# Kernel tuning notes

Hardware: AMD Instinct MI355X
Metric: run time of the kernel (lower is better)

## Reference

```python
import jax, jax.numpy as jnp
import numpy as np

B, L, HID, NH = 8, 1024, 1024, 16
DH = HID // NH
EPS = 1e-12


def _linear(x, W, b):
    # torch nn.Linear: y = x @ W.T + b
    return jnp.einsum('ble,oe->blo', x, W) + b


def _attend(qx, kx, vx, mask, Wq, bq, Wk, bk, Wv, bv):
    q = _linear(qx, Wq, bq).reshape(B, -1, NH, DH)
    k = _linear(kx, Wk, bk).reshape(B, -1, NH, DH)
    v = _linear(vx, Wv, bv).reshape(B, -1, NH, DH)
    scores = jnp.einsum('bqhd,bkhd->bhqk', q, k) / np.sqrt(DH).astype(np.float32)
    scores = scores + mask  # additive mask broadcast [B,1,1,Lk]
    probs = jax.nn.softmax(scores, axis=-1)  # dropout = identity (eval mode)
    ctx = jnp.einsum('bhqk,bkhd->bqhd', probs, v)
    return ctx.reshape(B, -1, HID)


def _layernorm(x, gamma, beta):
    mu = jnp.mean(x, axis=-1, keepdims=True)
    var = jnp.mean(jnp.square(x - mu), axis=-1, keepdims=True)
    return gamma * (x - mu) * jax.lax.rsqrt(var + EPS) + beta


def setup_inputs():
    key = jax.random.key(0)
    ks = jax.random.split(key, 20)
    s = 0.02
    d = {
        'cinput_tensor': jax.random.normal(ks[0], (B, L, HID), jnp.float32),
        'qinput_tensor': jax.random.normal(ks[1], (B, L, HID), jnp.float32),
        'attention_mask': jnp.zeros((B, 1, 1, L), jnp.float32),
        'qattention_mask': jnp.zeros((B, 1, 1, L), jnp.float32),
    }
    names = ['Wq', 'Wk', 'Wv', 'Wqq', 'Wqk', 'Wqv', 'Wo']
    for i, n in enumerate(names):
        d[n] = jax.random.normal(ks[2 + i], (HID, HID), jnp.float32) * s
        d['b' + n[1:]] = jnp.zeros((HID,), jnp.float32)
    d['gamma'] = jnp.ones((HID,), jnp.float32)
    d['beta'] = jnp.zeros((HID,), jnp.float32)
    return d


def reference(cinput_tensor, qinput_tensor, attention_mask, qattention_mask,
              Wq, bq, Wk, bk, Wv, bv, Wqq, bqq, Wqk, bqk, Wqv, bqv,
              Wo, bo, gamma, beta):
    enc, dec = cinput_tensor, qinput_tensor
    # c-branch: query from dec, key/value from enc
    ctx = _attend(dec, enc, enc, attention_mask, Wq, bq, Wk, bk, Wv, bv)
    # q-branch: query from enc, key/value from dec
    qctx = _attend(enc, dec, dec, qattention_mask, Wqq, bqq, Wqk, bqk, Wqv, bqv)
    # output: same dense/LayerNorm reused, and BOTH residuals add cinput_tensor
    # (faithful to the original module, including its apparent bug)
    c_out = _layernorm(_linear(ctx, Wo, bo) + cinput_tensor, gamma, beta)
    q_out = _layernorm(_linear(qctx, Wo, bo) + cinput_tensor, gamma, beta)
    return (c_out, q_out)
```

## Files before the change

kernel.cpp:

```cpp
#include <hip/hip_runtime.h>

typedef __bf16 bf16;
typedef unsigned short u16;
typedef __bf16 bf16x8 __attribute__((ext_vector_type(8)));
typedef __bf16 bf16x4 __attribute__((ext_vector_type(4)));
typedef float f32x4 __attribute__((ext_vector_type(4)));

#define GLD16(g, l) __builtin_amdgcn_global_load_lds( \
    (const __attribute__((address_space(1))) void*)(g), \
    (__attribute__((address_space(3))) void*)(l), 16, 0, 0)

#define MFMA_BF16 __builtin_amdgcn_mfma_f32_16x16x32_bf16

struct CvtFlat { const float* s[9]; bf16* d[9]; int off[10]; };

__global__ __launch_bounds__(256) void cvt_flat(CvtFlat a) {
  const int g = blockIdx.x * 256 + threadIdx.x;
  int seg = 0;
  #pragma unroll
  for (int i = 1; i < 9; ++i) seg += (g >= a.off[i]) ? 1 : 0;
  const int loc = (g - a.off[seg]) * 4;
  const f32x4 v = *(const f32x4*)(a.s[seg] + loc);
  bf16x4 o;
  #pragma unroll
  for (int j = 0; j < 4; ++j) o[j] = (bf16)v[j];
  *(bf16x4*)(a.d[seg] + loc) = o;
}

struct GemmDesc {
  const bf16* X;
  const bf16* W;
  const float* B;
  const float* R;
  bf16* Y;
  int vt;
};
struct GemmArgs { GemmDesc d[6]; };

__global__ __launch_bounds__(256, 2) void gemm128(GemmArgs args) {
  const GemmDesc g = args.d[blockIdx.z];
  __shared__ u16 As[128 * 64];
  __shared__ u16 Bs[128 * 64];
  const int tid = threadIdx.x;
  const int w = tid >> 6, lane = tid & 63;
  const int lq = lane >> 4, ll = lane & 15;
  const int lin = blockIdx.x + (blockIdx.y << 3);
  const int ntile = (lin >> 3) & 7;
  const int mtile = (lin & 7) | ((lin >> 6) << 3);
  const int m0 = mtile * 128, n0 = ntile * 128;
  const int wm = (w >> 1) * 64, wn = (w & 1) * 64;
  f32x4 acc[4][4] = {};

  for (int k0 = 0; k0 < 1024; k0 += 64) {
    #pragma unroll
    for (int i = 0; i < 4; ++i) {
      const int sb = w * 256 + i * 64;
      const int s = sb + lane;
      const int r = s >> 3, c = (s & 7) ^ (r & 7);
      GLD16(g.X + (m0 + r) * 1024 + k0 + c * 8, &As[sb * 8]);
      GLD16(g.W + (n0 + r) * 1024 + k0 + c * 8, &Bs[sb * 8]);
    }
    __syncthreads();
    #pragma unroll
    for (int kk = 0; kk < 64; kk += 32) {
      const int cb = (kk >> 3) + lq;
      bf16x8 a[4], b[4];
      #pragma unroll
      for (int t = 0; t < 4; ++t) {
        const int m = wm + t * 16 + ll;
        a[t] = *(const bf16x8*)&As[m * 64 + ((cb ^ (m & 7)) << 3)];
        const int n = wn + t * 16 + ll;
        b[t] = *(const bf16x8*)&Bs[n * 64 + ((cb ^ (n & 7)) << 3)];
      }
      #pragma unroll
      for (int mt = 0; mt < 4; ++mt)
        #pragma unroll
        for (int nt = 0; nt < 4; ++nt)
          acc[mt][nt] = MFMA_BF16(a[mt], b[nt], acc[mt][nt], 0, 0, 0);
    }
    __syncthreads();
  }

  float biasv[4];
  #pragma unroll
  for (int nt = 0; nt < 4; ++nt) biasv[nt] = g.B[n0 + wn + nt * 16 + ll];

  #pragma unroll
  for (int mt = 0; mt < 4; ++mt) {
    #pragma unroll
    for (int r = 0; r < 4; ++r) {
      const int m = m0 + wm + mt * 16 + lq * 4 + r;
      #pragma unroll
      for (int nt = 0; nt < 4; ++nt) {
        const int n = n0 + wn + nt * 16 + ll;
        float v = acc[mt][nt][r] + biasv[nt];
        if (g.R) v += g.R[m * 1024 + n];
        if (!g.vt) {
          g.Y[m * 1024 + n] = (bf16)v;
        } else {
          const int bb = m >> 10, tok = m & 1023;
          g.Y[(((bb << 4) + (n >> 6)) * 64 + (n & 63)) * 1024 + tok] = (bf16)v;
        }
      }
    }
  }
}

struct AttnDesc { const bf16* Qp; const bf16* Kp; const bf16* Vt; const float* mask; bf16* ctx; };

__global__ __launch_bounds__(256, 4) void attn_kernel(AttnDesc A0, AttnDesc A1) {
  const AttnDesc A = blockIdx.z ? A1 : A0;
  __shared__ u16 Ks[128 * 64];
  __shared__ u16 Vts[64 * 128];
  __shared__ u16 Pts[4 * 1024];
  const int tid = threadIdx.x;
  const int w = tid >> 6, lane = tid & 63;
  const int lq = lane >> 4, ll = lane & 15;
  const int lin = blockIdx.x + (blockIdx.y << 3);
  const int bh = (lin & 7) | ((lin >> 6) << 3);
  const int q0 = ((lin >> 3) & 7) * 128;
  const int b = bh >> 4, h = bh & 15;
  const float* mrow = A.mask + b * 1024;

  #pragma unroll
  for (int i = 0; i < 4; ++i) {
    const int sb = w * 256 + i * 64;
    const int s = sb + lane;
    const int r = s >> 3, c = (s & 7) ^ (r & 7);
    GLD16(A.Qp + (b * 1024 + q0 + r) * 1024 + h * 64 + c * 8, &Ks[sb * 8]);
  }
  __syncthreads();
  bf16x8 bq[2][2];
  #pragma unroll
  for (int nt = 0; nt < 2; ++nt)
    #pragma unroll
    for (int kd = 0; kd < 2; ++kd) {
      const int row = w * 32 + nt * 16 + ll;
      const int c8 = kd * 4 + lq;
      bq[nt][kd] = *(const bf16x8*)&Ks[row * 64 + ((c8 ^ (row & 7)) << 3)];
    }
  __syncthreads();

  f32x4 oacc[4][2] = {};
  float rsum[2] = {0.f, 0.f};

  for (int kt = 0; kt < 8; ++kt) {
    const int kk0 = kt * 128;
    #pragma unroll
    for (int i = 0; i < 4; ++i) {
      const int sb = w * 256 + i * 64;
      const int s = sb + lane;
      { const int r = s >> 3, c = (s & 7) ^ (r & 7);
        GLD16(A.Kp + (b * 1024 + kk0 + r) * 1024 + h * 64 + c * 8, &Ks[sb * 8]); }
      { const int r = s >> 4, c = (s & 15) ^ (r & 15);
        GLD16(A.Vt + (bh * 64 + r) * 1024 + kk0 + c * 8, &Vts[sb * 8]); }
    }
    __syncthreads();

    #pragma unroll
    for (int qtr = 0; qtr < 4; ++qtr) {
      bf16x8 ak[2][2];
      #pragma unroll
      for (int mh = 0; mh < 2; ++mh) {
        const int row = qtr * 32 + mh * 16 + ll;
        #pragma unroll
        for (int kd = 0; kd < 2; ++kd) {
          const int c8 = kd * 4 + lq;
          ak[mh][kd] = *(const bf16x8*)&Ks[row * 64 + ((c8 ^ (row & 7)) << 3)];
        }
      }
      f32x4 sacc[2][2] = {};
      #pragma unroll
      for (int mh = 0; mh < 2; ++mh)
        #pragma unroll
        for (int nt = 0; nt < 2; ++nt)
          #pragma unroll
          for (int kd = 0; kd < 2; ++kd)
            sacc[mh][nt] = MFMA_BF16(ak[mh][kd], bq[nt][kd], sacc[mh][nt], 0, 0, 0);

      f32x4 mv[2];
      #pragma unroll
      for (int mh = 0; mh < 2; ++mh)
        mv[mh] = *(const f32x4*)&mrow[kk0 + qtr * 32 + mh * 16 + lq * 4];

      #pragma unroll
      for (int mh = 0; mh < 2; ++mh)
        #pragma unroll
        for (int nt = 0; nt < 2; ++nt) {
          bf16x4 pv;
          #pragma unroll
          for (int rr = 0; rr < 4; ++rr) {
            const float p = __expf(fmaf(sacc[mh][nt][rr], 0.125f, mv[mh][rr]));
            rsum[nt] += p;
            pv[rr] = (bf16)p;
          }
          const int row = nt * 16 + ll;
          const int gq = mh * 2 + (lq >> 1);
          *(bf16x4*)&Pts[w * 1024 + row * 32 + ((gq ^ (row & 3)) << 3) + (lq & 1) * 4] = pv;
        }

      bf16x8 bp[2];
      #pragma unroll
      for (int nt = 0; nt < 2; ++nt) {
        const int row = nt * 16 + ll;
        bp[nt] = *(const bf16x8*)&Pts[w * 1024 + row * 32 + ((lq ^ (row & 3)) << 3)];
      }
      #pragma unroll
      for (int mtd = 0; mtd < 4; ++mtd) {
        const int row = mtd * 16 + ll;
        const int c16 = (qtr * 4 + lq) ^ (row & 15);
        const bf16x8 av = *(const bf16x8*)&Vts[row * 128 + (c16 << 3)];
        oacc[mtd][0] = MFMA_BF16(av, bp[0], oacc[mtd][0], 0, 0, 0);
        oacc[mtd][1] = MFMA_BF16(av, bp[1], oacc[mtd][1], 0, 0, 0);
      }
    }
    __syncthreads();
  }

  #pragma unroll
  for (int nt = 0; nt < 2; ++nt) {
    rsum[nt] += __shfl_xor(rsum[nt], 16, 64);
    rsum[nt] += __shfl_xor(rsum[nt], 32, 64);
  }

  #pragma unroll
  for (int nt = 0; nt < 2; ++nt) {
    const float inv = 1.f / rsum[nt];
    const int tok = q0 + w * 32 + nt * 16 + ll;
    #pragma unroll
    for (int mtd = 0; mtd < 4; ++mtd) {
      bf16x4 ov;
      #pragma unroll
      for (int rr = 0; rr < 4; ++rr) ov[rr] = (bf16)(oacc[mtd][nt][rr] * inv);
      *(bf16x4*)&A.ctx[(size_t)(b * 1024 + tok) * 1024 + h * 64 + mtd * 16 + lq * 4] = ov;
    }
  }
}

__global__ __launch_bounds__(256) void ln_kernel(const bf16* __restrict__ pre_c,
                                                 const bf16* __restrict__ pre_q,
                                                 const float* __restrict__ gamma,
                                                 const float* __restrict__ beta,
                                                 float* __restrict__ out) {
  const int row = blockIdx.x;
  const bf16* src = (row < 8192) ? (pre_c + (size_t)row * 1024)
                                 : (pre_q + (size_t)(row - 8192) * 1024);
  float* dst = out + (size_t)row * 1024;
  const int t = threadIdx.x;
  const bf16x4 xv = *(const bf16x4*)(src + t * 4);
  float x[4]; float s = 0.f, ss = 0.f;
  #pragma unroll
  for (int i = 0; i < 4; ++i) { x[i] = (float)xv[i]; s += x[i]; ss += x[i] * x[i]; }
  #pragma unroll
  for (int off = 1; off < 64; off <<= 1) { s += __shfl_xor(s, off, 64); ss += __shfl_xor(ss, off, 64); }
  __shared__ float red[8];
  const int w = t >> 6, lane = t & 63;
  if (lane == 0) { red[w * 2] = s; red[w * 2 + 1] = ss; }
  __syncthreads();
  s  = red[0] + red[2] + red[4] + red[6];
  ss = red[1] + red[3] + red[5] + red[7];
  const float mu = s * (1.f / 1024.f);
  float var = ss * (1.f / 1024.f) - mu * mu;
  var = fmaxf(var, 0.f);
  const float rs = rsqrtf(var + 1e-12f);
  const f32x4 gv = *(const f32x4*)(gamma + t * 4);
  const f32x4 bv = *(const f32x4*)(beta + t * 4);
  f32x4 yv;
  #pragma unroll
  for (int i = 0; i < 4; ++i) yv[i] = gv[i] * (x[i] - mu) * rs + bv[i];
  *(f32x4*)(dst + t * 4) = yv;
}

extern "C" void kernel_launch(void* const* d_in, const int* in_sizes, int n_in,
                              void* d_out, int out_size, void* d_ws, size_t ws_size,
                              hipStream_t stream) {
  const float* enc    = (const float*)d_in[0];
  const float* dec    = (const float*)d_in[1];
  const float* mask_c = (const float*)d_in[2];
  const float* mask_q = (const float*)d_in[3];
  const float* Wq  = (const float*)d_in[4];  const float* bq  = (const float*)d_in[5];
  const float* Wk  = (const float*)d_in[6];  const float* bk  = (const float*)d_in[7];
  const float* Wv  = (const float*)d_in[8];  const float* bv  = (const float*)d_in[9];
  const float* Wqq = (const float*)d_in[10]; const float* bqq = (const float*)d_in[11];
  const float* Wqk = (const float*)d_in[12]; const float* bqk = (const float*)d_in[13];
  const float* Wqv = (const float*)d_in[14]; const float* bqv = (const float*)d_in[15];
  const float* Wo  = (const float*)d_in[16]; const float* bo  = (const float*)d_in[17];
  const float* gamma = (const float*)d_in[18];
  const float* beta  = (const float*)d_in[19];
  float* out = (float*)d_out;

  bf16* ws = (bf16*)d_ws;
  const size_t XSZ = (size_t)8192 * 1024;
  const size_t WSZ = (size_t)1024 * 1024;
  bf16* enc_b = ws;
  bf16* dec_b = enc_b + XSZ;
  bf16* Wb[7];
  for (int i = 0; i < 7; ++i) Wb[i] = dec_b + XSZ + i * WSZ;
  bf16* after_w = Wb[6] + WSZ;

  CvtFlat ca;
  ca.s[0] = enc; ca.d[0] = enc_b;
  ca.s[1] = dec; ca.d[1] = dec_b;
  const float* Wsrc[7] = {Wq, Wk, Wv, Wqq, Wqk, Wqv, Wo};
  for (int i = 0; i < 7; ++i) { ca.s[2 + i] = Wsrc[i]; ca.d[2 + i] = Wb[i]; }
  int running = 0;
  const int segn[9] = {(int)(XSZ / 4), (int)(XSZ / 4), (int)(WSZ / 4), (int)(WSZ / 4),
                       (int)(WSZ / 4), (int)(WSZ / 4), (int)(WSZ / 4), (int)(WSZ / 4), (int)(WSZ / 4)};
  for (int i = 0; i < 9; ++i) { ca.off[i] = running; running += segn[i]; }
  ca.off[9] = running;
  const int cvt_blocks = running / 256;

  const size_t need_par = (size_t)(23 + 48) * 1024 * 1024 * 2;

  cvt_flat<<<dim3(cvt_blocks), 256, 0, stream>>>(ca);

  if (ws_size >= need_par) {
    bf16* Qc  = after_w;        bf16* Kc  = Qc + XSZ;  bf16* Vtc = Kc + XSZ;
    bf16* Qq  = Vtc + XSZ;      bf16* Kq  = Qq + XSZ;  bf16* Vtq = Kq + XSZ;
    bf16* ctx_c = enc_b;
    bf16* ctx_q = dec_b;
    bf16* pre_c = Qc;
    bf16* pre_q = Qq;

    GemmArgs pa = {};
    pa.d[0] = {dec_b, Wb[0], bq,  nullptr, Qc,  0};
    pa.d[1] = {enc_b, Wb[1], bk,  nullptr, Kc,  0};
    pa.d[2] = {enc_b, Wb[2], bv,  nullptr, Vtc, 1};
    pa.d[3] = {enc_b, Wb[3], bqq, nullptr, Qq,  0};
    pa.d[4] = {dec_b, Wb[4], bqk, nullptr, Kq,  0};
    pa.d[5] = {dec_b, Wb[5], bqv, nullptr, Vtq, 1};
    gemm128<<<dim3(8, 64, 6), 256, 0, stream>>>(pa);

    AttnDesc a0 = {Qc, Kc, Vtc, mask_c, ctx_c};
    AttnDesc a1 = {Qq, Kq, Vtq, mask_q, ctx_q};
    attn_kernel<<<dim3(8, 128, 2), 256, 0, stream>>>(a0, a1);

    GemmArgs oa = {};
    oa.d[0] = {ctx_c, Wb[6], bo, enc, pre_c, 0};
    oa.d[1] = {ctx_q, Wb[6], bo, enc, pre_q, 0};
    gemm128<<<dim3(8, 64, 2), 256, 0, stream>>>(oa);

    ln_kernel<<<dim3(16384), 256, 0, stream>>>(pre_c, pre_q, gamma, beta, out);
  } else {
    bf16* Q  = after_w;  bf16* K = Q + XSZ;  bf16* Vt = K + XSZ;
    bf16* ctx_c = Vt + XSZ;
    bf16* ctx_q = ctx_c + XSZ;
    bf16* pre_c = Q;
    bf16* pre_q = K;

    GemmArgs pa = {};
    pa.d[0] = {dec_b, Wb[0], bq,  nullptr, Q,  0};
    pa.d[1] = {enc_b, Wb[1], bk,  nullptr, K,  0};
    pa.d[2] = {enc_b, Wb[2], bv,  nullptr, Vt, 1};
    gemm128<<<dim3(8, 64, 3), 256, 0, stream>>>(pa);

    AttnDesc a0 = {Q, K, Vt, mask_c, ctx_c};
    attn_kernel<<<dim3(8, 128, 1), 256, 0, stream>>>(a0, a0);

    GemmArgs pb = {};
    pb.d[0] = {enc_b, Wb[3], bqq, nullptr, Q,  0};
    pb.d[1] = {dec_b, Wb[4], bqk, nullptr, K,  0};
    pb.d[2] = {dec_b, Wb[5], bqv, nullptr, Vt, 1};
    gemm128<<<dim3(8, 64, 3), 256, 0, stream>>>(pb);

    AttnDesc a1 = {Q, K, Vt, mask_q, ctx_q};
    attn_kernel<<<dim3(8, 128, 1), 256, 0, stream>>>(a1, a1);

    GemmArgs oa = {};
    oa.d[0] = {ctx_c, Wb[6], bo, enc, pre_c, 0};
    oa.d[1] = {ctx_q, Wb[6], bo, enc, pre_q, 0};
    gemm128<<<dim3(8, 64, 2), 256, 0, stream>>>(oa);

    ln_kernel<<<dim3(16384), 256, 0, stream>>>(pre_c, pre_q, gamma, beta, out);
  }
}
```

Before: 484.0 us.

## Replace 128x128 GEMM with 256x256 tile, 4-stage LDS pipelined kernel

Replaces the 128x128, 256-thread GEMM with a 256x256, 512-thread kernel. It uses a 4-slot shared-memory ring of K=32 slices, issuing global-to-LDS loads three slices ahead and interleaving them with MFMA bursts under raw barriers and explicit waitcnt. It also uses s_setprio around the MFMA bursts and a new swizzle and tile ordering. The goal is to hide global load latency and raise operand reuse per loaded byte. The cost is fewer blocks (128 tiles per matrix) with heavy register and LDS use (128KB LDS), which may limit occupancy and tail balance.

```diff
diff --git a/kernel.cpp b/kernel.cpp
--- a/kernel.cpp
+++ b/kernel.cpp
@@ -11,6 +11,9 @@
     (__attribute__((address_space(3))) void*)(l), 16, 0, 0)
 
 #define MFMA_BF16 __builtin_amdgcn_mfma_f32_16x16x32_bf16
+
+#define FENCE() asm volatile("" ::: "memory")
+#define BARRIER() do { FENCE(); __builtin_amdgcn_s_barrier(); FENCE(); } while (0)
 
 struct CvtFlat { const float* s[9]; bf16* d[9]; int off[10]; };
 
@@ -37,62 +40,115 @@
 };
 struct GemmArgs { GemmDesc d[6]; };
 
-__global__ __launch_bounds__(256, 2) void gemm128(GemmArgs args) {
+__device__ __forceinline__ void stage_slice(const bf16* G, int row0, int k0,
+                                            u16* slot, int w, int lane) {
+  #pragma unroll
+  for (int i = 0; i < 2; ++i) {
+    const int sb = i * 512 + w * 64;
+    const int s = sb + lane;
+    const int r = s >> 2, c = (s & 3) ^ ((r >> 1) & 3);
+    GLD16(G + (row0 + r) * 1024 + k0 + c * 8, &slot[sb * 8]);
+  }
+}
+
+template <bool STAGE, int VW>
+__device__ __forceinline__ void do_slice(
+    int sv, u16 (&As)[4][8192], u16 (&Bs)[4][8192], f32x4 (&acc)[8][4],
+    const int (&offA)[8], const int (&offB)[4],
+    const bf16* __restrict__ X, const bf16* __restrict__ W,
+    int m0, int n0, int w, int lane) {
+  const u16* Asl = &As[sv & 3][0];
+  const u16* Bsl = &Bs[sv & 3][0];
+  bf16x8 a[4], b[4];
+  #pragma unroll
+  for (int mt = 0; mt < 4; ++mt) a[mt] = *(const bf16x8*)&Asl[offA[mt]];
+  #pragma unroll
+  for (int nt = 0; nt < 4; ++nt) b[nt] = *(const bf16x8*)&Bsl[offB[nt]];
+  if constexpr (STAGE)
+    stage_slice(X, m0, (sv + 3) * 32, &As[(sv + 3) & 3][0], w, lane);
+  BARRIER();
+  asm volatile("s_waitcnt lgkmcnt(0)" ::: "memory");
+  __builtin_amdgcn_s_setprio(1);
+  #pragma unroll
+  for (int mt = 0; mt < 4; ++mt)
+    #pragma unroll
+    for (int nt = 0; nt < 4; ++nt)
+      acc[mt][nt] = MFMA_BF16(a[mt], b[nt], acc[mt][nt], 0, 0, 0);
+  __builtin_amdgcn_s_setprio(0);
+  BARRIER();
+  #pragma unroll
+  for (int mt = 0; mt < 4; ++mt) a[mt] = *(const bf16x8*)&Asl[offA[4 + mt]];
+  if constexpr (STAGE)
+    stage_slice(W, n0, (sv + 3) * 32, &Bs[(sv + 3) & 3][0], w, lane);
+  BARRIER();
+  asm volatile("s_waitcnt lgkmcnt(0)" ::: "memory");
+  __builtin_amdgcn_s_setprio(1);
+  #pragma unroll
+  for (int mt = 0; mt < 4; ++mt)
+    #pragma unroll
+    for (int nt = 0; nt < 4; ++nt)
+      acc[4 + mt][nt] = MFMA_BF16(a[mt], b[nt], acc[4 + mt][nt], 0, 0, 0);
+  __builtin_amdgcn_s_setprio(0);
+  if constexpr (VW == 8)      asm volatile("s_waitcnt vmcnt(8)" ::: "memory");
+  else if constexpr (VW == 4) asm volatile("s_waitcnt vmcnt(4)" ::: "memory");
+  else if constexpr (VW == 0) asm volatile("s_waitcnt vmcnt(0)" ::: "memory");
+  BARRIER();
+}
+
+__global__ __launch_bounds__(512, 2) void gemm256(GemmArgs args) {
   const GemmDesc g = args.d[blockIdx.z];
-  __shared__ u16 As[128 * 64];
-  __shared__ u16 Bs[128 * 64];
+  __shared__ u16 As[4][8192];
+  __shared__ u16 Bs[4][8192];
   const int tid = threadIdx.x;
   const int w = tid >> 6, lane = tid & 63;
   const int lq = lane >> 4, ll = lane & 15;
+  const int wr = w >> 2, wc = w & 3;
   const int lin = blockIdx.x + (blockIdx.y << 3);
-  const int ntile = (lin >> 3) & 7;
-  const int mtile = (lin & 7) | ((lin >> 6) << 3);
-  const int m0 = mtile * 128, n0 = ntile * 128;
-  const int wm = (w >> 1) * 64, wn = (w & 1) * 64;
-  f32x4 acc[4][4] = {};
-
-  for (int k0 = 0; k0 < 1024; k0 += 64) {
-    #pragma unroll
-    for (int i = 0; i < 4; ++i) {
-      const int sb = w * 256 + i * 64;
-      const int s = sb + lane;
-      const int r = s >> 3, c = (s & 7) ^ (r & 7);
-      GLD16(g.X + (m0 + r) * 1024 + k0 + c * 8, &As[sb * 8]);
-      GLD16(g.W + (n0 + r) * 1024 + k0 + c * 8, &Bs[sb * 8]);
-    }
-    __syncthreads();
-    #pragma unroll
-    for (int kk = 0; kk < 64; kk += 32) {
-      const int cb = (kk >> 3) + lq;
-      bf16x8 a[4], b[4];
-      #pragma unroll
-      for (int t = 0; t < 4; ++t) {
-        const int m = wm + t * 16 + ll;
-        a[t] = *(const bf16x8*)&As[m * 64 + ((cb ^ (m & 7)) << 3)];
-        const int n = wn + t * 16 + ll;
-        b[t] = *(const bf16x8*)&Bs[n * 64 + ((cb ^ (n & 7)) << 3)];
-      }
-      #pragma unroll
-      for (int mt = 0; mt < 4; ++mt)
-        #pragma unroll
-        for (int nt = 0; nt < 4; ++nt)
-          acc[mt][nt] = MFMA_BF16(a[mt], b[nt], acc[mt][nt], 0, 0, 0);
-    }
-    __syncthreads();
-  }
+  const int tile = (lin & 7) * 16 + (lin >> 3);
+  const int mtile = tile >> 2, ntile = tile & 3;
+  const int m0 = mtile * 256, n0 = ntile * 256;
+  f32x4 acc[8][4] = {};
+
+  int offA[8], offB[4];
+  #pragma unroll
+  for (int mt = 0; mt < 8; ++mt) {
+    const int am = wr * 128 + mt * 16 + ll;
+    offA[mt] = (am * 4 + (lq ^ ((am >> 1) & 3))) * 8;
+  }
+  #pragma unroll
+  for (int nt = 0; nt < 4; ++nt) {
+    const int bn = wc * 64 + nt * 16 + ll;
+    offB[nt] = (bn * 4 + (lq ^ ((bn >> 1) & 3))) * 8;
+  }
+
+  #pragma unroll
+  for (int ss = 0; ss < 3; ++ss) {
+    stage_slice(g.X, m0, ss * 32, &As[ss][0], w, lane);
+    stage_slice(g.W, n0, ss * 32, &Bs[ss][0], w, lane);
+  }
+  asm volatile("s_waitcnt vmcnt(8)" ::: "memory");
+  BARRIER();
+
+  #pragma unroll 4
+  for (int s = 0; s < 28; ++s)
+    do_slice<true, 8>(s, As, Bs, acc, offA, offB, g.X, g.W, m0, n0, w, lane);
+  do_slice<true, 8>(28, As, Bs, acc, offA, offB, g.X, g.W, m0, n0, w, lane);
+  do_slice<false, 4>(29, As, Bs, acc, offA, offB, g.X, g.W, m0, n0, w, lane);
+  do_slice<false, 0>(30, As, Bs, acc, offA, offB, g.X, g.W, m0, n0, w, lane);
+  do_slice<false, -1>(31, As, Bs, acc, offA, offB, g.X, g.W, m0, n0, w, lane);
 
   float biasv[4];
   #pragma unroll
-  for (int nt = 0; nt < 4; ++nt) biasv[nt] = g.B[n0 + wn + nt * 16 + ll];
-
-  #pragma unroll
-  for (int mt = 0; mt < 4; ++mt) {
+  for (int nt = 0; nt < 4; ++nt) biasv[nt] = g.B[n0 + wc * 64 + nt * 16 + ll];
+
+  #pragma unroll
+  for (int mt = 0; mt < 8; ++mt) {
     #pragma unroll
     for (int r = 0; r < 4; ++r) {
-      const int m = m0 + wm + mt * 16 + lq * 4 + r;
+      const int m = m0 + wr * 128 + mt * 16 + lq * 4 + r;
       #pragma unroll
       for (int nt = 0; nt < 4; ++nt) {
-        const int n = n0 + wn + nt * 16 + ll;
+        const int n = n0 + wc * 64 + nt * 16 + ll;
         float v = acc[mt][nt][r] + biasv[nt];
         if (g.R) v += g.R[m * 1024 + n];
         if (!g.vt) {
@@ -329,7 +385,7 @@
     pa.d[3] = {enc_b, Wb[3], bqq, nullptr, Qq,  0};
     pa.d[4] = {dec_b, Wb[4], bqk, nullptr, Kq,  0};
     pa.d[5] = {dec_b, Wb[5], bqv, nullptr, Vtq, 1};
-    gemm128<<<dim3(8, 64, 6), 256, 0, stream>>>(pa);
+    gemm256<<<dim3(8, 16, 6), 512, 0, stream>>>(pa);
 
     AttnDesc a0 = {Qc, Kc, Vtc, mask_c, ctx_c};
     AttnDesc a1 = {Qq, Kq, Vtq, mask_q, ctx_q};
@@ -338,7 +394,7 @@
     GemmArgs oa = {};
     oa.d[0] = {ctx_c, Wb[6], bo, enc, pre_c, 0};
     oa.d[1] = {ctx_q, Wb[6], bo, enc, pre_q, 0};
-    gemm128<<<dim3(8, 64, 2), 256, 0, stream>>>(oa);
+    gemm256<<<dim3(8, 16, 2), 512, 0, stream>>>(oa);
 
     ln_kernel<<<dim3(16384), 256, 0, stream>>>(pre_c, pre_q, gamma, beta, out);
   } else {
@@ -352,7 +408,7 @@
     pa.d[0] = {dec_b, Wb[0], bq,  nullptr, Q,  0};
     pa.d[1] = {enc_b, Wb[1], bk,  nullptr, K,  0};
     pa.d[2] = {enc_b, Wb[2], bv,  nullptr, Vt, 1};
-    gemm128<<<dim3(8, 64, 3), 256, 0, stream>>>(pa);
+    gemm256<<<dim3(8, 16, 3), 512, 0, stream>>>(pa);
 
     AttnDesc a0 = {Q, K, Vt, mask_c, ctx_c};
     attn_kernel<<<dim3(8, 128, 1), 256, 0, stream>>>(a0, a0);
@@ -361,7 +417,7 @@
     pb.d[0] = {enc_b, Wb[3], bqq, nullptr, Q,  0};
     pb.d[1] = {dec_b, Wb[4], bqk, nullptr, K,  0};
     pb.d[2] = {dec_b, Wb[5], bqv, nullptr, Vt, 1};
-    gemm128<<<dim3(8, 64, 3), 256, 0, stream>>>(pb);
+    gemm256<<<dim3(8, 16, 3), 512, 0, stream>>>(pb);
 
     AttnDesc a1 = {Q, K, Vt, mask_q, ctx_q};
     attn_kernel<<<dim3(8, 128, 1), 256, 0, stream>>>(a1, a1);
@@ -369,7 +425,7 @@
     GemmArgs oa = {};
     oa.d[0] = {ctx_c, Wb[6], bo, enc, pre_c, 0};
     oa.d[1] = {ctx_q, Wb[6], bo, enc, pre_q, 0};
-    gemm128<<<dim3(8, 64, 2), 256, 0, stream>>>(oa);
+    gemm256<<<dim3(8, 16, 2), 512, 0, stream>>>(oa);
 
     ln_kernel<<<dim3(16384), 256, 0, stream>>>(pre_c, pre_q, gamma, beta, out);
   }
```

Result: slower. 535.3 us (+10.6%).

## Double-buffer K/V tiles in attention kernel with async prefetch of next tile

Applied to the files above, without the earlier changes.

Splits the key loop into 16 tiles of 64 keys and double-buffers K and V^T in shared memory, so the next tile's global-to-LDS loads are issued before computing on the current one. It uses manual vmcnt waits and raw barriers instead of __syncthreads. Mask values are hoisted so they load ahead of the wait. The aim is to hide global load latency behind MFMA work. The cost is more barriers per key, smaller tiles, and reliance on exact vmcnt counting being correct.

```diff
diff --git a/kernel.cpp b/kernel.cpp
--- a/kernel.cpp
+++ b/kernel.cpp
@@ -11,6 +11,9 @@
     (__attribute__((address_space(3))) void*)(l), 16, 0, 0)
 
 #define MFMA_BF16 __builtin_amdgcn_mfma_f32_16x16x32_bf16
+
+#define FENCE() asm volatile("" ::: "memory")
+#define BARRIER() do { FENCE(); __builtin_amdgcn_s_barrier(); FENCE(); } while (0)
 
 struct CvtFlat { const float* s[9]; bf16* d[9]; int off[10]; };
 
@@ -110,8 +113,8 @@
 
 __global__ __launch_bounds__(256, 4) void attn_kernel(AttnDesc A0, AttnDesc A1) {
   const AttnDesc A = blockIdx.z ? A1 : A0;
-  __shared__ u16 Ks[128 * 64];
-  __shared__ u16 Vts[64 * 128];
+  __shared__ u16 Ks[2 * 64 * 64];
+  __shared__ u16 Vts[2 * 64 * 64];
   __shared__ u16 Pts[4 * 1024];
   const int tid = threadIdx.x;
   const int w = tid >> 6, lane = tid & 63;
@@ -141,24 +144,44 @@
     }
   __syncthreads();
 
+  auto stage_kv = [&](int kt) {
+    const int kk0 = kt << 6;
+    const int db = (kt & 1) << 12;
+    #pragma unroll
+    for (int i = 0; i < 2; ++i) {
+      const int sb = i * 256 + w * 64;
+      const int s = sb + lane;
+      const int r = s >> 3, c = (s & 7) ^ (r & 7);
+      GLD16(A.Kp + (b * 1024 + kk0 + r) * 1024 + h * 64 + c * 8, &Ks[db + sb * 8]);
+      GLD16(A.Vt + ((bh << 6) + r) * 1024 + kk0 + c * 8, &Vts[db + sb * 8]);
+    }
+  };
+
   f32x4 oacc[4][2] = {};
   float rsum[2] = {0.f, 0.f};
 
-  for (int kt = 0; kt < 8; ++kt) {
-    const int kk0 = kt * 128;
-    #pragma unroll
-    for (int i = 0; i < 4; ++i) {
-      const int sb = w * 256 + i * 64;
-      const int s = sb + lane;
-      { const int r = s >> 3, c = (s & 7) ^ (r & 7);
-        GLD16(A.Kp + (b * 1024 + kk0 + r) * 1024 + h * 64 + c * 8, &Ks[sb * 8]); }
-      { const int r = s >> 4, c = (s & 15) ^ (r & 15);
-        GLD16(A.Vt + (bh * 64 + r) * 1024 + kk0 + c * 8, &Vts[sb * 8]); }
-    }
-    __syncthreads();
-
-    #pragma unroll
-    for (int qtr = 0; qtr < 4; ++qtr) {
+  stage_kv(0);
+
+  for (int kt = 0; kt < 16; ++kt) {
+    const int kk0 = kt << 6;
+    const int db = (kt & 1) << 12;
+    f32x4 mvk[2][2];
+    #pragma unroll
+    for (int qtr = 0; qtr < 2; ++qtr)
+      #pragma unroll
+      for (int mh = 0; mh < 2; ++mh)
+        mvk[qtr][mh] = *(const f32x4*)&mrow[kk0 + qtr * 32 + mh * 16 + lq * 4];
+    FENCE();
+    if (kt < 15) {
+      stage_kv(kt + 1);
+      asm volatile("s_waitcnt vmcnt(8)" ::: "memory");
+    } else {
+      asm volatile("s_waitcnt vmcnt(4)" ::: "memory");
+    }
+    BARRIER();
+
+    #pragma unroll
+    for (int qtr = 0; qtr < 2; ++qtr) {
       bf16x8 ak[2][2];
       #pragma unroll
       for (int mh = 0; mh < 2; ++mh) {
@@ -166,7 +189,7 @@
         #pragma unroll
         for (int kd = 0; kd < 2; ++kd) {
           const int c8 = kd * 4 + lq;
-          ak[mh][kd] = *(const bf16x8*)&Ks[row * 64 + ((c8 ^ (row & 7)) << 3)];
+          ak[mh][kd] = *(const bf16x8*)&Ks[db + row * 64 + ((c8 ^ (row & 7)) << 3)];
         }
       }
       f32x4 sacc[2][2] = {};
@@ -178,11 +201,6 @@
           for (int kd = 0; kd < 2; ++kd)
             sacc[mh][nt] = MFMA_BF16(ak[mh][kd], bq[nt][kd], sacc[mh][nt], 0, 0, 0);
 
-      f32x4 mv[2];
-      #pragma unroll
-      for (int mh = 0; mh < 2; ++mh)
-        mv[mh] = *(const f32x4*)&mrow[kk0 + qtr * 32 + mh * 16 + lq * 4];
-
       #pragma unroll
       for (int mh = 0; mh < 2; ++mh)
         #pragma unroll
@@ -190,7 +208,7 @@
           bf16x4 pv;
           #pragma unroll
           for (int rr = 0; rr < 4; ++rr) {
-            const float p = __expf(fmaf(sacc[mh][nt][rr], 0.125f, mv[mh][rr]));
+            const float p = __expf(fmaf(sacc[mh][nt][rr], 0.125f, mvk[qtr][mh][rr]));
             rsum[nt] += p;
             pv[rr] = (bf16)p;
           }
@@ -208,13 +226,13 @@
       #pragma unroll
       for (int mtd = 0; mtd < 4; ++mtd) {
         const int row = mtd * 16 + ll;
-        const int c16 = (qtr * 4 + lq) ^ (row & 15);
-        const bf16x8 av = *(const bf16x8*)&Vts[row * 128 + (c16 << 3)];
+        const int c8v = ((qtr << 2) + lq) ^ (row & 7);
+        const bf16x8 av = *(const bf16x8*)&Vts[db + row * 64 + (c8v << 3)];
         oacc[mtd][0] = MFMA_BF16(av, bp[0], oacc[mtd][0], 0, 0, 0);
         oacc[mtd][1] = MFMA_BF16(av, bp[1], oacc[mtd][1], 0, 0, 0);
       }
     }
-    __syncthreads();
+    BARRIER();
   }
 
   #pragma unroll
```

After: 470.6 us. -2.8%, faster.
